# Optimization experiments

Hardware: AMD Instinct MI355X
Metric: run time of the kernel (lower is better)

Reference implementation:

```python
import jax, jax.numpy as jnp
import numpy as np

E = 1024
H = 8
D = E // H
WINDOW = 256
EPS = 1e-5


def layernorm(x, w, b):
    mu = jnp.mean(x, axis=-1, keepdims=True)
    var = jnp.mean((x - mu) ** 2, axis=-1, keepdims=True)
    return (x - mu) * jax.lax.rsqrt(var + EPS) * w + b


def setup_inputs() -> dict:
    key = jax.random.key(0)
    ks = jax.random.split(key, 12)
    B, T = 2, 2048
    s = 1.0 / np.sqrt(E)
    return {
        "x": jax.random.normal(ks[0], (B, T, E), jnp.float32),
        "ln1_w": jnp.ones((E,), jnp.float32),
        "ln1_b": jnp.zeros((E,), jnp.float32),
        "ln2_w": jnp.ones((E,), jnp.float32),
        "ln2_b": jnp.zeros((E,), jnp.float32),
        "in_proj_w": jax.random.normal(ks[1], (3 * E, E), jnp.float32) * s,
        "in_proj_b": jnp.zeros((3 * E,), jnp.float32),
        "out_w": jax.random.normal(ks[2], (E, E), jnp.float32) * s,
        "out_b": jnp.zeros((E,), jnp.float32),
        "w1": jax.random.normal(ks[3], (4 * E, E), jnp.float32) * s,
        "b1": jnp.zeros((4 * E,), jnp.float32),
        "w2": jax.random.normal(ks[4], (E, 4 * E), jnp.float32) * (1.0 / np.sqrt(4 * E)),
        "b2": jnp.zeros((E,), jnp.float32),
    }


def reference(x, ln1_w, ln1_b, ln2_w, ln2_b, in_proj_w, in_proj_b, out_w, out_b, w1, b1, w2, b2):
    B, T, _ = x.shape
    h = layernorm(x, ln1_w, ln1_b)
    # qkv projection: torch Linear is x @ W.T + b
    qkv = h @ in_proj_w.T + in_proj_b  # [B,T,3E]
    q, k, v = jnp.split(qkv, 3, axis=-1)
    q = q.reshape(B, T, H, D).transpose(0, 2, 1, 3)  # [B,H,T,D]
    k = k.reshape(B, T, H, D).transpose(0, 2, 1, 3)
    v = v.reshape(B, T, H, D).transpose(0, 2, 1, 3)
    scores = jnp.einsum("bhqd,bhkd->bhqk", q, k) / np.sqrt(D)
    idx = jnp.arange(T)
    row = idx[:, None]
    col = idx[None, :]
    # masked where future (col>row) OR outside window (col < row - WINDOW)
    allowed = (col <= row) & (col >= row - WINDOW)
    scores = jnp.where(allowed, scores, -jnp.inf)
    attn = jax.nn.softmax(scores, axis=-1)
    out = jnp.einsum("bhqk,bhkd->bhqd", attn, v)  # [B,H,T,D]
    out = out.transpose(0, 2, 1, 3).reshape(B, T, E)
    out = out @ out_w.T + out_b
    h2 = x + out
    m = layernorm(h2, ln2_w, ln2_b)
    m = jax.nn.relu(m @ w1.T + b1) @ w2.T + b2
    return h2 + m
```

## Files before the change

### kernel.cpp

```cpp
#include <hip/hip_runtime.h>

#define TOK 4096
#define EMB 1024

typedef __attribute__((ext_vector_type(8))) short s16x8;
typedef __attribute__((ext_vector_type(4))) float f32x4;

__device__ __forceinline__ unsigned short f2bf(float f) {
  union { float f; unsigned int u; } v; v.f = f;
  unsigned int r = v.u + 0x7FFFu + ((v.u >> 16) & 1u);
  return (unsigned short)(r >> 16);
}
__device__ __forceinline__ float bf2f(unsigned short u) {
  union { unsigned int u; float f; } v; v.u = ((unsigned int)u) << 16; return v.f;
}

#define GLOAD_LDS16(g, l) __builtin_amdgcn_global_load_lds( \
    (const __attribute__((address_space(1))) void*)(g), \
    (__attribute__((address_space(3))) void*)(l), 16, 0, 0)

template<int RELU, int PART, int NT>
__global__ __launch_bounds__(512)
void gemm256(const unsigned short* __restrict__ A,
             const unsigned short* __restrict__ B,
             const float* __restrict__ bias,
             unsigned short* __restrict__ C, int M, int N, int K)
{
  __shared__ unsigned short lds[2][2][128 * 128];
  const int tid = threadIdx.x;
  const int lane = tid & 63;
  const int w = tid >> 6;
  const int wr = w >> 2, wc = w & 3;
  const int l15 = lane & 15, lhi = lane >> 4;
  const int nbm = M >> 8;
  const int bm = blockIdx.x % nbm, bn = blockIdx.x / nbm;
  const int m0 = bm << 8, n0 = bn << 8;
  const int k0 = blockIdx.y * (NT * 64);

  const char* Abase = (const char*)(A + (size_t)m0 * K) + (size_t)k0 * 2;
  const char* Bbase = (const char*)(B + (size_t)n0 * K) + (size_t)k0 * 2;
  const size_t rowb = (size_t)K * 2;

  const int srt = tid >> 3;
  const int sccx = ((tid & 7) << 4) ^ ((srt & 7) << 4);
  const char* gA = Abase + (size_t)srt * rowb + sccx;
  const char* gB = Bbase + (size_t)srt * rowb + sccx;

  auto STAGE_A = [&](int ktl, int h, int p) {
    char* d = (char*)&lds[0][0][0] + p * 32768 + h * 16384 + (w << 10);
    const char* g = gA + (size_t)(h * 128) * rowb + ktl * 128;
    GLOAD_LDS16(g, d);
    GLOAD_LDS16(g + 64 * rowb, d + 8192);
  };
  auto STAGE_B = [&](int ktl, int h, int p) {
    char* d = (char*)&lds[1][0][0] + p * 32768 + h * 16384 + (w << 10);
    const char* g = gB + (size_t)(h * 128) * rowb + ktl * 128;
    GLOAD_LDS16(g, d);
    GLOAD_LDS16(g + 64 * rowb, d + 8192);
  };

  const int rdxor = (l15 & 7) << 4;
  const char* pA0 = (const char*)&lds[0][0][0] + (wr * 128 + l15) * 128 + ((0 * 64 + lhi * 16) ^ rdxor);
  const char* pA1 = (const char*)&lds[0][0][0] + (wr * 128 + l15) * 128 + ((1 * 64 + lhi * 16) ^ rdxor);
  const char* pB0 = (const char*)&lds[1][0][0] + (wc * 64 + l15) * 128 + ((0 * 64 + lhi * 16) ^ rdxor);
  const char* pB1 = (const char*)&lds[1][0][0] + (wc * 64 + l15) * 128 + ((1 * 64 + lhi * 16) ^ rdxor);

  f32x4 acc[8][4];
#pragma unroll
  for (int mf = 0; mf < 8; ++mf)
#pragma unroll
    for (int nf = 0; nf < 4; ++nf)
#pragma unroll
      for (int j = 0; j < 4; ++j) acc[mf][nf][j] = 0.f;

  STAGE_A(0, 0, 0); STAGE_A(0, 1, 0);
  STAGE_B(0, 0, 0); STAGE_B(0, 1, 0);
  STAGE_A(1, 0, 1); STAGE_A(1, 1, 1);
  STAGE_B(1, 0, 1);
  asm volatile("s_waitcnt vmcnt(6)" ::: "memory");
  __builtin_amdgcn_s_barrier();

  s16x8 af[8][2], bf[4][2];

#pragma unroll
  for (int kt = 0; kt < NT; ++kt) {
    const int P = (kt & 1) << 15;
    const int p = kt & 1;

#pragma unroll
    for (int mi = 0; mi < 4; ++mi) {
      af[mi][0] = *(const s16x8*)(pA0 + mi * 2048 + P);
      af[mi][1] = *(const s16x8*)(pA1 + mi * 2048 + P);
    }
#pragma unroll
    for (int ni = 0; ni < 2; ++ni) {
      bf[ni][0] = *(const s16x8*)(pB0 + ni * 2048 + P);
      bf[ni][1] = *(const s16x8*)(pB1 + ni * 2048 + P);
    }
#pragma unroll
    for (int mi = 4; mi < 8; ++mi) {
      af[mi][0] = *(const s16x8*)(pA0 + mi * 2048 + P);
      af[mi][1] = *(const s16x8*)(pA1 + mi * 2048 + P);
    }
#pragma unroll
    for (int ni = 2; ni < 4; ++ni) {
      bf[ni][0] = *(const s16x8*)(pB0 + ni * 2048 + P);
      bf[ni][1] = *(const s16x8*)(pB1 + ni * 2048 + P);
    }

    if (kt + 1 < NT) STAGE_B(kt + 1, 1, p ^ 1);

    __builtin_amdgcn_s_setprio(1);
#pragma unroll
    for (int mi = 0; mi < 4; ++mi)
#pragma unroll
      for (int ni = 0; ni < 2; ++ni)
#pragma unroll
        for (int ks = 0; ks < 2; ++ks)
          acc[mi][ni] = __builtin_amdgcn_mfma_f32_16x16x32_bf16(af[mi][ks], bf[ni][ks], acc[mi][ni], 0, 0, 0);
#pragma unroll
    for (int mi = 4; mi < 8; ++mi)
#pragma unroll
      for (int ni = 0; ni < 2; ++ni)
#pragma unroll
        for (int ks = 0; ks < 2; ++ks)
          acc[mi][ni] = __builtin_amdgcn_mfma_f32_16x16x32_bf16(af[mi][ks], bf[ni][ks], acc[mi][ni], 0, 0, 0);
#pragma unroll
    for (int mi = 0; mi < 4; ++mi)
#pragma unroll
      for (int ni = 2; ni < 4; ++ni)
#pragma unroll
        for (int ks = 0; ks < 2; ++ks)
          acc[mi][ni] = __builtin_amdgcn_mfma_f32_16x16x32_bf16(af[mi][ks], bf[ni][ks], acc[mi][ni], 0, 0, 0);
#pragma unroll
    for (int mi = 4; mi < 8; ++mi)
#pragma unroll
      for (int ni = 2; ni < 4; ++ni)
#pragma unroll
        for (int ks = 0; ks < 2; ++ks)
          acc[mi][ni] = __builtin_amdgcn_mfma_f32_16x16x32_bf16(af[mi][ks], bf[ni][ks], acc[mi][ni], 0, 0, 0);
    __builtin_amdgcn_s_setprio(0);

    __builtin_amdgcn_s_barrier();

    if (kt + 2 < NT) {
      STAGE_A(kt + 2, 0, p);
      STAGE_A(kt + 2, 1, p);
      STAGE_B(kt + 2, 0, p);
    }

    if (kt + 1 < NT) {
      if (kt + 2 < NT) asm volatile("s_waitcnt vmcnt(6)" ::: "memory");
      else             asm volatile("s_waitcnt vmcnt(0)" ::: "memory");
      __builtin_amdgcn_s_barrier();
    }
  }

  unsigned short* Cw = PART ? C + (size_t)blockIdx.y * M * N : C;
#pragma unroll
  for (int mf = 0; mf < 8; ++mf) {
    const int row = m0 + wr * 128 + mf * 16 + lhi * 4;
#pragma unroll
    for (int nf = 0; nf < 4; ++nf) {
      const int col = n0 + wc * 64 + nf * 16 + l15;
      const float bv = PART ? 0.f : bias[col];
#pragma unroll
      for (int j = 0; j < 4; ++j) {
        float v = acc[mf][nf][j] + bv;
        if (RELU) v = fmaxf(v, 0.f);
        Cw[(size_t)(row + j) * N + col] = f2bf(v);
      }
    }
  }
}

__global__ __launch_bounds__(256)
void reduce_add(const unsigned short* __restrict__ part, const unsigned short* __restrict__ res,
                const float* __restrict__ bias, float* __restrict__ out,
                int MN, int N, int S)
{
  const int i4 = (blockIdx.x * 256 + threadIdx.x) * 4;
  if (i4 >= MN) return;
  const int col = i4 & (N - 1);
  const ushort4 r = *(const ushort4*)(res + i4);
  float4 v;
  v.x = bf2f(r.x) + bias[col];
  v.y = bf2f(r.y) + bias[col + 1];
  v.z = bf2f(r.z) + bias[col + 2];
  v.w = bf2f(r.w) + bias[col + 3];
  for (int s = 0; s < S; ++s) {
    const ushort4 p = *(const ushort4*)(part + (size_t)s * MN + i4);
    v.x += bf2f(p.x); v.y += bf2f(p.y); v.z += bf2f(p.z); v.w += bf2f(p.w);
  }
  *(float4*)(out + i4) = v;
}

__global__ __launch_bounds__(256)
void reduce_ln(const unsigned short* __restrict__ part, const float* __restrict__ x,
               const float* __restrict__ ob, const float* __restrict__ ln_w,
               const float* __restrict__ ln_b, unsigned short* __restrict__ h2,
               unsigned short* __restrict__ m_in, int S)
{
  const int row = blockIdx.x;
  const int t = threadIdx.x;
  const size_t off = (size_t)row * EMB + t * 4;
  float4 v = *(const float4*)(x + off);
  const float4 obv = ((const float4*)ob)[t];
  v.x += obv.x; v.y += obv.y; v.z += obv.z; v.w += obv.w;
  for (int s = 0; s < S; ++s) {
    const ushort4 p = *(const ushort4*)(part + (size_t)s * TOK * EMB + off);
    v.x += bf2f(p.x); v.y += bf2f(p.y); v.z += bf2f(p.z); v.w += bf2f(p.w);
  }
  ushort4 hb;
  hb.x = f2bf(v.x); hb.y = f2bf(v.y); hb.z = f2bf(v.z); hb.w = f2bf(v.w);
  *(ushort4*)(h2 + off) = hb;

  float s1 = v.x + v.y + v.z + v.w;
  float s2 = v.x * v.x + v.y * v.y + v.z * v.z + v.w * v.w;
#pragma unroll
  for (int o = 1; o < 64; o <<= 1) { s1 += __shfl_xor(s1, o); s2 += __shfl_xor(s2, o); }
  __shared__ float red[8];
  if ((t & 63) == 0) { red[t >> 6] = s1; red[4 + (t >> 6)] = s2; }
  __syncthreads();
  s1 = red[0] + red[1] + red[2] + red[3];
  s2 = red[4] + red[5] + red[6] + red[7];
  const float mu = s1 * (1.f / EMB);
  const float rs = rsqrtf(s2 * (1.f / EMB) - mu * mu + 1e-5f);
  const float4 wv = ((const float4*)ln_w)[t];
  const float4 bv = ((const float4*)ln_b)[t];
  ushort4 o;
  o.x = f2bf((v.x - mu) * rs * wv.x + bv.x);
  o.y = f2bf((v.y - mu) * rs * wv.y + bv.y);
  o.z = f2bf((v.z - mu) * rs * wv.z + bv.z);
  o.w = f2bf((v.w - mu) * rs * wv.w + bv.w);
  ((ushort4*)(m_in + (size_t)row * EMB))[t] = o;
}

__global__ __launch_bounds__(256)
void ln_bf16(const float* __restrict__ x, const float* __restrict__ wt,
             const float* __restrict__ bs, unsigned short* __restrict__ out)
{
  const int row = blockIdx.x;
  const int t = threadIdx.x;
  const float4 v = ((const float4*)(x + (size_t)row * EMB))[t];
  float s = v.x + v.y + v.z + v.w;
  float s2 = v.x * v.x + v.y * v.y + v.z * v.z + v.w * v.w;
#pragma unroll
  for (int off = 1; off < 64; off <<= 1) { s += __shfl_xor(s, off); s2 += __shfl_xor(s2, off); }
  __shared__ float red[8];
  if ((t & 63) == 0) { red[t >> 6] = s; red[4 + (t >> 6)] = s2; }
  __syncthreads();
  s = red[0] + red[1] + red[2] + red[3];
  s2 = red[4] + red[5] + red[6] + red[7];
  const float mu = s * (1.f / EMB);
  const float rs = rsqrtf(s2 * (1.f / EMB) - mu * mu + 1e-5f);
  const float4 wv = ((const float4*)wt)[t];
  const float4 bv = ((const float4*)bs)[t];
  ushort4 o;
  o.x = f2bf((v.x - mu) * rs * wv.x + bv.x);
  o.y = f2bf((v.y - mu) * rs * wv.y + bv.y);
  o.z = f2bf((v.z - mu) * rs * wv.z + bv.z);
  o.w = f2bf((v.w - mu) * rs * wv.w + bv.w);
  ((ushort4*)(out + (size_t)row * EMB))[t] = o;
}

#define Q0 786432
#define Q1 (Q0 + 262144)
#define Q2 (Q1 + 1048576)
#define Q3 (Q2 + 1048576)
__global__ __launch_bounds__(256)
void cvt4(const float* __restrict__ s0, const float* __restrict__ s1,
          const float* __restrict__ s2, const float* __restrict__ s3,
          unsigned short* __restrict__ d0, unsigned short* __restrict__ d1,
          unsigned short* __restrict__ d2, unsigned short* __restrict__ d3)
{
  const int i = blockIdx.x * 256 + threadIdx.x;
  const float* s; unsigned short* d; int off;
  if (i < Q0)      { s = s0; d = d0; off = i; }
  else if (i < Q1) { s = s1; d = d1; off = i - Q0; }
  else if (i < Q2) { s = s2; d = d2; off = i - Q1; }
  else             { s = s3; d = d3; off = i - Q2; }
  const float4 v = ((const float4*)s)[off];
  ushort4 o;
  o.x = f2bf(v.x); o.y = f2bf(v.y); o.z = f2bf(v.z); o.w = f2bf(v.w);
  ((ushort4*)d)[off] = o;
}

__global__ __launch_bounds__(256)
void attn_win(const unsigned short* __restrict__ qkv, unsigned short* __restrict__ aout)
{
  __shared__ unsigned short Ks[64 * 136];
  __shared__ unsigned short Vt[128 * 72];
  __shared__ unsigned short Ps[4 * 16 * 72];
  const int bh = blockIdx.y;
  const int b = bh >> 3, hh = bh & 7;
  const int q0 = blockIdx.x << 6;
  const int tid = threadIdx.x, lane = tid & 63, w = tid >> 6;
  const int l15 = lane & 15, lhi = lane >> 4;
  const size_t base = (size_t)b * 2048 * 3072;

  s16x8 qf[4];
  {
    const unsigned short* qp = qkv + base + (size_t)(q0 + w * 16 + l15) * 3072 + hh * 128 + lhi * 8;
#pragma unroll
    for (int ks = 0; ks < 4; ++ks) qf[ks] = *(const s16x8*)(qp + ks * 32);
  }

  f32x4 o[8];
#pragma unroll
  for (int n = 0; n < 8; ++n)
#pragma unroll
    for (int j = 0; j < 4; ++j) o[n][j] = 0.f;
  float mrow[4] = {-1e30f, -1e30f, -1e30f, -1e30f};
  float lrow[4] = {0.f, 0.f, 0.f, 0.f};

  for (int t = 0; t < 5; ++t) {
    const int kt0 = q0 - 256 + t * 64;
    if (kt0 < 0) continue;
    __syncthreads();
    {
      const unsigned short* kg = qkv + base + (size_t)kt0 * 3072 + 1024 + hh * 128;
#pragma unroll
      for (int i = 0; i < 4; ++i) {
        const int c = tid + i * 256;
        const int r = c >> 4, cc = (c & 15) << 3;
        *(s16x8*)(Ks + r * 136 + cc) = *(const s16x8*)(kg + (size_t)r * 3072 + cc);
      }
      const unsigned short* vg = qkv + base + (size_t)kt0 * 3072 + 2048 + hh * 128;
#pragma unroll
      for (int i = 0; i < 2; ++i) {
        const int c = tid + i * 256;
        const int r2 = c >> 4, cc = (c & 15) << 3;
        s16x8 v0 = *(const s16x8*)(vg + (size_t)(2 * r2) * 3072 + cc);
        s16x8 v1 = *(const s16x8*)(vg + (size_t)(2 * r2 + 1) * 3072 + cc);
#pragma unroll
        for (int jj = 0; jj < 8; ++jj) {
          unsigned int pk = (unsigned int)(unsigned short)v0[jj] |
                            ((unsigned int)(unsigned short)v1[jj] << 16);
          *(unsigned int*)(Vt + (cc + jj) * 72 + 2 * r2) = pk;
        }
      }
    }
    __syncthreads();

    f32x4 s[4];
#pragma unroll
    for (int n = 0; n < 4; ++n)
#pragma unroll
      for (int j = 0; j < 4; ++j) s[n][j] = 0.f;
#pragma unroll
    for (int ks = 0; ks < 4; ++ks) {
#pragma unroll
      for (int n = 0; n < 4; ++n) {
        s16x8 kf = *(const s16x8*)(Ks + (n * 16 + l15) * 136 + ks * 32 + lhi * 8);
        s[n] = __builtin_amdgcn_mfma_f32_16x16x32_bf16(qf[ks], kf, s[n], 0, 0, 0);
      }
    }
    const bool mlo = (t == 0);
    const bool mhi = (kt0 == q0);
#pragma unroll
    for (int n = 0; n < 4; ++n) {
      const int kcol = n * 16 + l15;
#pragma unroll
      for (int j = 0; j < 4; ++j) {
        const int qrow = w * 16 + lhi * 4 + j;
        float v = s[n][j] * 0.08838834764831845f;
        if ((mlo && kcol < qrow) || (mhi && kcol > qrow)) v = -1e30f;
        s[n][j] = v;
      }
    }
    float alpha[4];
#pragma unroll
    for (int j = 0; j < 4; ++j) {
      float mx = fmaxf(fmaxf(s[0][j], s[1][j]), fmaxf(s[2][j], s[3][j]));
#pragma unroll
      for (int off = 1; off < 16; off <<= 1) mx = fmaxf(mx, __shfl_xor(mx, off));
      const float mn = fmaxf(mrow[j], mx);
      alpha[j] = __expf(mrow[j] - mn);
      mrow[j] = mn;
    }
    float rowsum[4] = {0.f, 0.f, 0.f, 0.f};
#pragma unroll
    for (int n = 0; n < 4; ++n)
#pragma unroll
      for (int j = 0; j < 4; ++j) {
        const float p = __expf(s[n][j] - mrow[j]);
        rowsum[j] += p;
        Ps[(w * 16 + lhi * 4 + j) * 72 + n * 16 + l15] = f2bf(p);
      }
#pragma unroll
    for (int j = 0; j < 4; ++j) {
      float rs = rowsum[j];
#pragma unroll
      for (int off = 1; off < 16; off <<= 1) rs += __shfl_xor(rs, off);
      lrow[j] = lrow[j] * alpha[j] + rs;
    }
#pragma unroll
    for (int n = 0; n < 8; ++n)
#pragma unroll
      for (int j = 0; j < 4; ++j) o[n][j] *= alpha[j];
#pragma unroll
    for (int ks = 0; ks < 2; ++ks) {
      const s16x8 pf = *(const s16x8*)(Ps + (w * 16 + l15) * 72 + ks * 32 + lhi * 8);
#pragma unroll
      for (int n = 0; n < 8; ++n) {
        const s16x8 vf = *(const s16x8*)(Vt + (n * 16 + l15) * 72 + ks * 32 + lhi * 8);
        o[n] = __builtin_amdgcn_mfma_f32_16x16x32_bf16(pf, vf, o[n], 0, 0, 0);
      }
    }
  }
  unsigned short* op = aout + (size_t)(b * 2048 + q0 + w * 16) * 1024 + hh * 128;
#pragma unroll
  for (int n = 0; n < 8; ++n)
#pragma unroll
    for (int j = 0; j < 4; ++j)
      op[(size_t)(lhi * 4 + j) * 1024 + n * 16 + l15] = f2bf(o[n][j] / lrow[j]);
}

extern "C" void kernel_launch(void* const* d_in, const int* in_sizes, int n_in,
                              void* d_out, int out_size, void* d_ws, size_t ws_size,
                              hipStream_t stream)
{
  (void)in_sizes; (void)n_in; (void)out_size; (void)ws_size;
  const float* x         = (const float*)d_in[0];
  const float* ln1_w     = (const float*)d_in[1];
  const float* ln1_b     = (const float*)d_in[2];
  const float* ln2_w     = (const float*)d_in[3];
  const float* ln2_b     = (const float*)d_in[4];
  const float* in_proj_w = (const float*)d_in[5];
  const float* in_proj_b = (const float*)d_in[6];
  const float* out_w     = (const float*)d_in[7];
  const float* out_b     = (const float*)d_in[8];
  const float* w1        = (const float*)d_in[9];
  const float* b1        = (const float*)d_in[10];
  const float* w2        = (const float*)d_in[11];
  const float* b2        = (const float*)d_in[12];
  float* out = (float*)d_out;

  char* ws = (char*)d_ws;
  unsigned short* h    = (unsigned short*)(ws);
  unsigned short* wqkv = (unsigned short*)(ws + (8u << 20));
  unsigned short* wout = (unsigned short*)(ws + (14u << 20));
  unsigned short* w1b  = (unsigned short*)(ws + (16u << 20));
  unsigned short* w2b  = (unsigned short*)(ws + (24u << 20));
  unsigned short* qkv  = (unsigned short*)(ws + (32u << 20));
  unsigned short* aout = (unsigned short*)(ws + (56u << 20));
  unsigned short* h2   = (unsigned short*)(ws + (64u << 20));
  unsigned short* m_in = (unsigned short*)(ws + (80u << 20));
  unsigned short* act  = (unsigned short*)(ws + (88u << 20));
  unsigned short* part_op = (unsigned short*)(ws + (88u << 20));
  unsigned short* part_m2 = (unsigned short*)(ws + (32u << 20));

  cvt4<<<dim3(Q3 / 256), 256, 0, stream>>>(in_proj_w, out_w, w1, w2, wqkv, wout, w1b, w2b);
  ln_bf16<<<dim3(TOK), 256, 0, stream>>>(x, ln1_w, ln1_b, h);

  gemm256<0, 0, 16><<<dim3(16 * 12), 512, 0, stream>>>(h, wqkv, in_proj_b, qkv, 4096, 3072, 1024);
  attn_win<<<dim3(32, 16), 256, 0, stream>>>(qkv, aout);

  gemm256<0, 1, 4><<<dim3(16 * 4, 4), 512, 0, stream>>>(aout, wout, nullptr, part_op, 4096, 1024, 1024);
  reduce_ln<<<dim3(TOK), 256, 0, stream>>>(part_op, x, out_b, ln2_w, ln2_b, h2, m_in, 4);

  gemm256<1, 0, 16><<<dim3(16 * 16), 512, 0, stream>>>(m_in, w1b, b1, act, 4096, 4096, 1024);

  gemm256<0, 1, 16><<<dim3(16 * 4, 4), 512, 0, stream>>>(act, w2b, nullptr, part_m2, 4096, 1024, 4096);
  reduce_add<<<dim3(4096 * 1024 / 4 / 256), 256, 0, stream>>>(part_m2, h2, b2, out, 4096 * 1024, 1024, 4);
}
```

Baseline: 189.7 us.

## Fuse split-K reduction into final GEMM via grid sync; merge weight cast and LN1

Merges the weight-conversion kernel and the first layernorm into a single prep launch. Folds the final split-K reduce-add into the last FFN GEMM, which now runs as a cooperative launch with a grid-wide sync before each thread reduces the partials and writes the fp32 output. The goal is to remove two kernel launches and their inter-kernel gaps. The cost is a grid barrier and a cooperative launch whose 256 blocks of 512 threads must all be co-resident.

```diff
diff --git a/kernel.cpp b/kernel.cpp
--- a/kernel.cpp
+++ b/kernel.cpp
@@ -1,4 +1,5 @@
 #include <hip/hip_runtime.h>
+#include <hip/hip_cooperative_groups.h>
 
 #define TOK 4096
 #define EMB 1024
@@ -19,12 +20,13 @@
     (const __attribute__((address_space(1))) void*)(g), \
     (__attribute__((address_space(3))) void*)(l), 16, 0, 0)
 
-template<int RELU, int PART, int NT>
+template<int RELU, int PART, int NT, int FRED>
 __global__ __launch_bounds__(512)
 void gemm256(const unsigned short* __restrict__ A,
              const unsigned short* __restrict__ B,
              const float* __restrict__ bias,
-             unsigned short* __restrict__ C, int M, int N, int K)
+             unsigned short* __restrict__ C, int M, int N, int K,
+             const unsigned short* __restrict__ res, float* __restrict__ outF)
 {
   __shared__ unsigned short lds[2][2][128 * 128];
   const int tid = threadIdx.x;
@@ -163,7 +165,7 @@
 #pragma unroll
     for (int nf = 0; nf < 4; ++nf) {
       const int col = n0 + wc * 64 + nf * 16 + l15;
-      const float bv = PART ? 0.f : bias[col];
+      const float bv = (PART || FRED) ? 0.f : bias[col];
 #pragma unroll
       for (int j = 0; j < 4; ++j) {
         float v = acc[mf][nf][j] + bv;
@@ -172,27 +174,32 @@
       }
     }
   }
-}
-
-__global__ __launch_bounds__(256)
-void reduce_add(const unsigned short* __restrict__ part, const unsigned short* __restrict__ res,
-                const float* __restrict__ bias, float* __restrict__ out,
-                int MN, int N, int S)
-{
-  const int i4 = (blockIdx.x * 256 + threadIdx.x) * 4;
-  if (i4 >= MN) return;
-  const int col = i4 & (N - 1);
-  const ushort4 r = *(const ushort4*)(res + i4);
-  float4 v;
-  v.x = bf2f(r.x) + bias[col];
-  v.y = bf2f(r.y) + bias[col + 1];
-  v.z = bf2f(r.z) + bias[col + 2];
-  v.w = bf2f(r.w) + bias[col + 3];
-  for (int s = 0; s < S; ++s) {
-    const ushort4 p = *(const ushort4*)(part + (size_t)s * MN + i4);
-    v.x += bf2f(p.x); v.y += bf2f(p.y); v.z += bf2f(p.z); v.w += bf2f(p.w);
-  }
-  *(float4*)(out + i4) = v;
+
+  if constexpr (FRED != 0) {
+    __threadfence();
+    cooperative_groups::this_grid().sync();
+    __threadfence();
+    const int gq = (int)((blockIdx.y * gridDim.x + blockIdx.x) * 512 + tid);
+    const int nthr = (int)(gridDim.x * gridDim.y * 512);
+    const int quads = (M * N) >> 2;
+    const size_t MN = (size_t)M * N;
+    for (int q = gq; q < quads; q += nthr) {
+      const int i4 = q << 2;
+      const int col = i4 & (N - 1);
+      const ushort4 r = *(const ushort4*)(res + i4);
+      float4 v;
+      v.x = bf2f(r.x) + bias[col];
+      v.y = bf2f(r.y) + bias[col + 1];
+      v.z = bf2f(r.z) + bias[col + 2];
+      v.w = bf2f(r.w) + bias[col + 3];
+#pragma unroll
+      for (int s = 0; s < 4; ++s) {
+        const ushort4 pp = *(const ushort4*)(C + s * MN + i4);
+        v.x += bf2f(pp.x); v.y += bf2f(pp.y); v.z += bf2f(pp.z); v.w += bf2f(pp.w);
+      }
+      *(float4*)(outF + i4) = v;
+    }
+  }
 }
 
 __global__ __launch_bounds__(256)
@@ -216,16 +223,16 @@
   *(ushort4*)(h2 + off) = hb;
 
   float s1 = v.x + v.y + v.z + v.w;
-  float s2 = v.x * v.x + v.y * v.y + v.z * v.z + v.w * v.w;
-#pragma unroll
-  for (int o = 1; o < 64; o <<= 1) { s1 += __shfl_xor(s1, o); s2 += __shfl_xor(s2, o); }
+  float sq = v.x * v.x + v.y * v.y + v.z * v.z + v.w * v.w;
+#pragma unroll
+  for (int o = 1; o < 64; o <<= 1) { s1 += __shfl_xor(s1, o); sq += __shfl_xor(sq, o); }
   __shared__ float red[8];
-  if ((t & 63) == 0) { red[t >> 6] = s1; red[4 + (t >> 6)] = s2; }
+  if ((t & 63) == 0) { red[t >> 6] = s1; red[4 + (t >> 6)] = sq; }
   __syncthreads();
   s1 = red[0] + red[1] + red[2] + red[3];
-  s2 = red[4] + red[5] + red[6] + red[7];
+  sq = red[4] + red[5] + red[6] + red[7];
   const float mu = s1 * (1.f / EMB);
-  const float rs = rsqrtf(s2 * (1.f / EMB) - mu * mu + 1e-5f);
+  const float rs = rsqrtf(sq * (1.f / EMB) - mu * mu + 1e-5f);
   const float4 wv = ((const float4*)ln_w)[t];
   const float4 bv = ((const float4*)ln_b)[t];
   ushort4 o;
@@ -236,54 +243,55 @@
   ((ushort4*)(m_in + (size_t)row * EMB))[t] = o;
 }
 
+#define Q0 786432
+#define Q1 (Q0 + 262144)
+#define Q2 (Q1 + 1048576)
+#define Q3 (Q2 + 1048576)
+#define CVT_BLOCKS (Q3 / 256)
 __global__ __launch_bounds__(256)
-void ln_bf16(const float* __restrict__ x, const float* __restrict__ wt,
-             const float* __restrict__ bs, unsigned short* __restrict__ out)
+void prep(const float* __restrict__ w0, const float* __restrict__ w1s,
+          const float* __restrict__ w2s, const float* __restrict__ w3s,
+          unsigned short* __restrict__ d0, unsigned short* __restrict__ d1,
+          unsigned short* __restrict__ d2, unsigned short* __restrict__ d3,
+          const float* __restrict__ x, const float* __restrict__ ln_w,
+          const float* __restrict__ ln_b, unsigned short* __restrict__ h)
 {
-  const int row = blockIdx.x;
+  __shared__ float red[8];
+  const int bid = blockIdx.x;
   const int t = threadIdx.x;
+  if (bid < CVT_BLOCKS) {
+    const int i = bid * 256 + t;
+    const float* s; unsigned short* d; int off;
+    if (i < Q0)      { s = w0;  d = d0; off = i; }
+    else if (i < Q1) { s = w1s; d = d1; off = i - Q0; }
+    else if (i < Q2) { s = w2s; d = d2; off = i - Q1; }
+    else             { s = w3s; d = d3; off = i - Q2; }
+    const float4 v = ((const float4*)s)[off];
+    ushort4 o;
+    o.x = f2bf(v.x); o.y = f2bf(v.y); o.z = f2bf(v.z); o.w = f2bf(v.w);
+    ((ushort4*)d)[off] = o;
+    return;
+  }
+  const int row = bid - CVT_BLOCKS;
   const float4 v = ((const float4*)(x + (size_t)row * EMB))[t];
-  float s = v.x + v.y + v.z + v.w;
-  float s2 = v.x * v.x + v.y * v.y + v.z * v.z + v.w * v.w;
-#pragma unroll
-  for (int off = 1; off < 64; off <<= 1) { s += __shfl_xor(s, off); s2 += __shfl_xor(s2, off); }
-  __shared__ float red[8];
-  if ((t & 63) == 0) { red[t >> 6] = s; red[4 + (t >> 6)] = s2; }
+  float sm = v.x + v.y + v.z + v.w;
+  float sq = v.x * v.x + v.y * v.y + v.z * v.z + v.w * v.w;
+#pragma unroll
+  for (int off = 1; off < 64; off <<= 1) { sm += __shfl_xor(sm, off); sq += __shfl_xor(sq, off); }
+  if ((t & 63) == 0) { red[t >> 6] = sm; red[4 + (t >> 6)] = sq; }
   __syncthreads();
-  s = red[0] + red[1] + red[2] + red[3];
-  s2 = red[4] + red[5] + red[6] + red[7];
-  const float mu = s * (1.f / EMB);
-  const float rs = rsqrtf(s2 * (1.f / EMB) - mu * mu + 1e-5f);
-  const float4 wv = ((const float4*)wt)[t];
-  const float4 bv = ((const float4*)bs)[t];
+  sm = red[0] + red[1] + red[2] + red[3];
+  sq = red[4] + red[5] + red[6] + red[7];
+  const float mu = sm * (1.f / EMB);
+  const float rs = rsqrtf(sq * (1.f / EMB) - mu * mu + 1e-5f);
+  const float4 wv = ((const float4*)ln_w)[t];
+  const float4 bv = ((const float4*)ln_b)[t];
   ushort4 o;
   o.x = f2bf((v.x - mu) * rs * wv.x + bv.x);
   o.y = f2bf((v.y - mu) * rs * wv.y + bv.y);
   o.z = f2bf((v.z - mu) * rs * wv.z + bv.z);
   o.w = f2bf((v.w - mu) * rs * wv.w + bv.w);
-  ((ushort4*)(out + (size_t)row * EMB))[t] = o;
-}
-
-#define Q0 786432
-#define Q1 (Q0 + 262144)
-#define Q2 (Q1 + 1048576)
-#define Q3 (Q2 + 1048576)
-__global__ __launch_bounds__(256)
-void cvt4(const float* __restrict__ s0, const float* __restrict__ s1,
-          const float* __restrict__ s2, const float* __restrict__ s3,
-          unsigned short* __restrict__ d0, unsigned short* __restrict__ d1,
-          unsigned short* __restrict__ d2, unsigned short* __restrict__ d3)
-{
-  const int i = blockIdx.x * 256 + threadIdx.x;
-  const float* s; unsigned short* d; int off;
-  if (i < Q0)      { s = s0; d = d0; off = i; }
-  else if (i < Q1) { s = s1; d = d1; off = i - Q0; }
-  else if (i < Q2) { s = s2; d = d2; off = i - Q1; }
-  else             { s = s3; d = d3; off = i - Q2; }
-  const float4 v = ((const float4*)s)[off];
-  ushort4 o;
-  o.x = f2bf(v.x); o.y = f2bf(v.y); o.z = f2bf(v.z); o.w = f2bf(v.w);
-  ((ushort4*)d)[off] = o;
+  ((ushort4*)(h + (size_t)row * EMB))[t] = o;
 }
 
 __global__ __launch_bounds__(256)
@@ -451,17 +459,33 @@
   unsigned short* part_op = (unsigned short*)(ws + (88u << 20));
   unsigned short* part_m2 = (unsigned short*)(ws + (32u << 20));
 
-  cvt4<<<dim3(Q3 / 256), 256, 0, stream>>>(in_proj_w, out_w, w1, w2, wqkv, wout, w1b, w2b);
-  ln_bf16<<<dim3(TOK), 256, 0, stream>>>(x, ln1_w, ln1_b, h);
-
-  gemm256<0, 0, 16><<<dim3(16 * 12), 512, 0, stream>>>(h, wqkv, in_proj_b, qkv, 4096, 3072, 1024);
+  prep<<<dim3(CVT_BLOCKS + TOK), 256, 0, stream>>>(
+      in_proj_w, out_w, w1, w2, wqkv, wout, w1b, w2b, x, ln1_w, ln1_b, h);
+
+  gemm256<0, 0, 16, 0><<<dim3(16 * 12), 512, 0, stream>>>(
+      h, wqkv, in_proj_b, qkv, 4096, 3072, 1024, nullptr, nullptr);
+
   attn_win<<<dim3(32, 16), 256, 0, stream>>>(qkv, aout);
 
-  gemm256<0, 1, 4><<<dim3(16 * 4, 4), 512, 0, stream>>>(aout, wout, nullptr, part_op, 4096, 1024, 1024);
+  gemm256<0, 1, 4, 0><<<dim3(16 * 4, 4), 512, 0, stream>>>(
+      aout, wout, nullptr, part_op, 4096, 1024, 1024, nullptr, nullptr);
+
   reduce_ln<<<dim3(TOK), 256, 0, stream>>>(part_op, x, out_b, ln2_w, ln2_b, h2, m_in, 4);
 
-  gemm256<1, 0, 16><<<dim3(16 * 16), 512, 0, stream>>>(m_in, w1b, b1, act, 4096, 4096, 1024);
-
-  gemm256<0, 1, 16><<<dim3(16 * 4, 4), 512, 0, stream>>>(act, w2b, nullptr, part_m2, 4096, 1024, 4096);
-  reduce_add<<<dim3(4096 * 1024 / 4 / 256), 256, 0, stream>>>(part_m2, h2, b2, out, 4096 * 1024, 1024, 4);
-}
+  gemm256<1, 0, 16, 0><<<dim3(16 * 16), 512, 0, stream>>>(
+      m_in, w1b, b1, act, 4096, 4096, 1024, nullptr, nullptr);
+
+  {
+    const unsigned short* a_ = act;
+    const unsigned short* b_ = w2b;
+    const float* bias_ = b2;
+    unsigned short* c_ = part_m2;
+    int M_ = 4096, N_ = 1024, K_ = 4096;
+    const unsigned short* res_ = h2;
+    float* out_ = out;
+    void* args[] = {(void*)&a_, (void*)&b_, (void*)&bias_, (void*)&c_,
+                    (void*)&M_, (void*)&N_, (void*)&K_, (void*)&res_, (void*)&out_};
+    (void)hipLaunchCooperativeKernel((void*)gemm256<0, 1, 16, 1>, dim3(16 * 4, 4),
+                                     dim3(512), args, 0, stream);
+  }
+}
```

New measurement: 335.0 us. 76.6% more time.
